# Performance work log

Hardware: AMD Instinct MI355X
Metric: run time of the kernel (lower is better)

The kernel has to match this reference:

```python
import jax, jax.numpy as jnp
import numpy as np

N_NODES = 50000
N_EDGES_UND = 400000
N_GRAPHS = 128
LATENT = 64
OUT_DIM = 64
NODE_F = 64
EDGE_F = 32
MAX_LV = 3


def setup_inputs() -> dict:
    key = jax.random.key(0)
    ks = jax.random.split(key, 12)
    rng = np.random.default_rng(0)
    # Build consistent directed edge list: each undirected pair (u,v) yields
    # directed edges e (u->v) and e+E_und (v->u); rev maps each to its twin.
    u = rng.integers(0, N_NODES, size=N_EDGES_UND)
    v = rng.integers(0, N_NODES, size=N_EDGES_UND)
    src = jnp.asarray(np.concatenate([u, v]), dtype=jnp.int32)
    dst = jnp.asarray(np.concatenate([v, u]), dtype=jnp.int32)
    e = np.arange(N_EDGES_UND)
    rev = jnp.asarray(np.concatenate([e + N_EDGES_UND, e]), dtype=jnp.int32)
    graph_ids = jnp.sort(jax.random.randint(ks[0], (N_NODES,), 0, N_GRAPHS)).astype(jnp.int32)
    s = 0.05
    return {
        'node_feat': jax.random.normal(ks[1], (N_NODES, NODE_F), jnp.float32),
        'edge_feat': jax.random.normal(ks[2], (2 * N_EDGES_UND, EDGE_F), jnp.float32),
        'src': src, 'dst': dst, 'rev': rev,
        'graph_ids': graph_ids, 'n_graphs': N_GRAPHS,
        'Wn': jax.random.normal(ks[3], (NODE_F, LATENT), jnp.float32) * s,
        'bn': jnp.zeros((LATENT,), jnp.float32),
        'We': jax.random.normal(ks[4], (EDGE_F, LATENT), jnp.float32) * s,
        'be': jnp.zeros((LATENT,), jnp.float32),
        'Wc': jax.random.normal(ks[5], (LATENT, LATENT), jnp.float32) * s,
        'bc': jnp.zeros((LATENT,), jnp.float32),
        'Wo': jax.random.normal(ks[6], (LATENT, OUT_DIM), jnp.float32) * s,
        'bo': jnp.zeros((OUT_DIM,), jnp.float32),
    }


def reference(node_feat, edge_feat, src, dst, rev, graph_ids, n_graphs,
              Wn, bn, We, be, Wc, bc, Wo, bo):
    n_nodes = node_feat.shape[0]
    # w_n2l / w_e2l
    input_node_linear = node_feat @ Wn + bn                  # [N, D]
    input_edge_linear = edge_feat @ We + be                  # [E, D]
    # n2e spmm: each directed edge gathers its source node's row
    input_message = input_edge_linear + input_node_linear[src]  # [E, D]
    cur = jax.nn.relu(input_message)
    # loopy BP: e2e spmm = (sum of messages into src node) - reverse-edge message
    for _ in range(MAX_LV):
        node_agg = jax.ops.segment_sum(cur, dst, num_segments=n_nodes)  # [N, D]
        e2epool = node_agg[src] - cur[rev]                              # [E, D]
        cur = jax.nn.relu(e2epool @ Wc + bc + input_message)
    # e2n spmm: sum incoming edge messages per node
    e2npool = jax.ops.segment_sum(cur, dst, num_segments=n_nodes)       # [N, D]
    hidden_msg = jax.nn.relu(e2npool)
    reluact = jax.nn.relu(hidden_msg @ Wo + bo)                         # [N, out]
    # subg spmm: sum node outputs per graph
    y = jax.ops.segment_sum(reluact, graph_ids, num_segments=n_graphs)  # [G, out]
    return jax.nn.relu(y)
```

## Files before the change

### kernel.cpp

```cpp
#include <hip/hip_runtime.h>


#define NN 50000
#define NE 800000
#define NG 128
#define D 64
#define LDE 36
#define LDW 66
#define LDO 72

typedef unsigned short u16;
typedef unsigned int u32;
typedef __bf16 bf16x8 __attribute__((ext_vector_type(8)));
typedef float f32x4 __attribute__((ext_vector_type(4)));
typedef short s16x2 __attribute__((ext_vector_type(2)));

__device__ __forceinline__ float b2f(u16 u){ u32 x=((u32)u)<<16; float f; __builtin_memcpy(&f,&x,4); return f; }
__device__ __forceinline__ u16 f2b(float f){ u32 x; __builtin_memcpy(&x,&f,4); x += 0x7fffu + ((x>>16)&1u); return (u16)(x>>16); }
__device__ __forceinline__ u32 pack2(float a, float b){ return (u32)f2b(a) | ((u32)f2b(b)<<16); }
__device__ __forceinline__ void unpack8(uint4 v, float* o){
  o[0]=b2f((u16)(v.x&0xffffu)); o[1]=b2f((u16)(v.x>>16));
  o[2]=b2f((u16)(v.y&0xffffu)); o[3]=b2f((u16)(v.y>>16));
  o[4]=b2f((u16)(v.z&0xffffu)); o[5]=b2f((u16)(v.z>>16));
  o[6]=b2f((u16)(v.w&0xffffu)); o[7]=b2f((u16)(v.w>>16));
}
__device__ __forceinline__ void atomic_pk_bf16(u16* addr, float lo, float hi){
  s16x2 v; v.x = (short)f2b(lo); v.y = (short)f2b(hi);
  __builtin_amdgcn_global_atomic_fadd_v2bf16((s16x2*)addr, v);
}

__global__ __launch_bounds__(256) void k_prep(const float* __restrict__ Wc, const float* __restrict__ We,
                                              u16* __restrict__ wcB, u16* __restrict__ weB){
  int i = blockIdx.x*256 + threadIdx.x;
  if (i < 4096){
    int nt = i>>10, r = i&1023;
    int h = r>>9, r2 = r&511;
    int j = r2>>3, kk = r2&7;
    int row = nt*16 + (j&15);
    int k = h*32 + (j>>4)*8 + kk;
    wcB[i] = f2b(Wc[k*D + row]);
  }
  int t = i - 4096;
  if (t >= 0 && t < 2048){
    int nt = t>>9, r = t&511;
    int j = r>>3, kk = r&7;
    int row = nt*16 + (j&15);
    int k = (j>>4)*8 + kk;
    weB[t] = f2b(We[k*D + row]);
  }
}

__global__ __launch_bounds__(256) void k_inl(const float* __restrict__ nf, const float* __restrict__ Wn,
                                             const float* __restrict__ bn, u16* __restrict__ inlb){
  __shared__ float w[D*D];
  for (int i=threadIdx.x;i<D*D;i+=256) w[i]=Wn[i];
  __syncthreads();
  const int d = threadIdx.x&63;
  const int n = blockIdx.x*4 + (threadIdx.x>>6);
  if (n>=NN) return;
  float v = bn[d];
  const float* row = nf + (size_t)n*D;
  #pragma unroll 8
  for (int k=0;k<D;k++) v += row[k]*w[k*D+d];
  inlb[(size_t)n*D+d] = f2b(v);
}

__global__ __launch_bounds__(256) void k_im(const float* __restrict__ ef, const u16* __restrict__ weB,
                                            const float* __restrict__ be, const u16* __restrict__ inlb,
                                            const int* __restrict__ src, const int* __restrict__ perm,
                                            u16* __restrict__ imP){
  __shared__ __align__(16) u16 efs[64*LDE];
  __shared__ float os[64*68];
  const int t = threadIdx.x;
  const int ebase = blockIdx.x*64;
  {
    int e=t>>2, k0=(t&3)*8;
    const float* p = ef + (size_t)(ebase+e)*32 + k0;
    float4 v0=*(const float4*)p, v1=*(const float4*)(p+4);
    uint4 pk = make_uint4(pack2(v0.x,v0.y),pack2(v0.z,v0.w),pack2(v1.x,v1.y),pack2(v1.z,v1.w));
    *(uint4*)&efs[e*LDE + k0] = pk;
  }
  {
    int w=t>>6, lane=t&63, q=lane>>4, mr=lane&15;
    int rowb=w*16;
    bf16x8 A = *(const bf16x8*)&efs[(rowb+mr)*LDE + q*8];
    #pragma unroll
    for (int nt=0;nt<4;nt++){
      bf16x8 B = *(const bf16x8*)(weB + nt*512 + lane*8);
      f32x4 acc = {0.f,0.f,0.f,0.f};
      acc = __builtin_amdgcn_mfma_f32_16x16x32_bf16(A,B,acc,0,0,0);
      #pragma unroll
      for (int r=0;r<4;r++) os[(rowb+q*4+r)*68 + nt*16+mr] = acc[r];
    }
  }
  {
    int e=t>>2, d0=(t&3)*16;
    const size_t eg = (size_t)(ebase+e);
    const int s = src[eg], ps = perm[eg];
    const u16* ip = inlb + (size_t)s*D + d0;
    uint4 iv0 = *(const uint4*)ip, iv1 = *(const uint4*)(ip+8);
    float il[16]; unpack8(iv0,il); unpack8(iv1,il+8);
    float x[16];
    #pragma unroll
    for (int j=0;j<16;j++) x[j] = os[e*68 + d0 + j] + be[d0+j] + il[j];
    uint4 p0 = make_uint4(pack2(x[0],x[1]),pack2(x[2],x[3]),pack2(x[4],x[5]),pack2(x[6],x[7]));
    uint4 p1 = make_uint4(pack2(x[8],x[9]),pack2(x[10],x[11]),pack2(x[12],x[13]),pack2(x[14],x[15]));
    u16* op = imP + (size_t)ps*D + d0;
    *(uint4*)op = p0; *(uint4*)(op+8) = p1;
  }
}

template<int MODE>
__global__ __launch_bounds__(256) void k_iter(const u16* __restrict__ imP, const u16* __restrict__ revIn,
      const u16* __restrict__ naWb, const u16* __restrict__ wcB, const float* __restrict__ bc,
      const int* __restrict__ srcP, const int* __restrict__ prevP, const int* __restrict__ nodeP,
      u16* __restrict__ revOut, u16* __restrict__ naWb_out){
  __shared__ __align__(16) u16 xs[64*LDW];
  __shared__ __align__(16) u16 os[64*LDO];
  __shared__ int nid[64];
  const int t = threadIdx.x;
  const int lane = t&63, w = t>>6;
  const size_t sbase = (size_t)blockIdx.x*64;
  if (lane < 16) nid[w*16 + lane] = nodeP[sbase + w*16 + lane];
  {
    const int e = t>>2, d0 = (t&3)*16;
    const size_t slot = sbase + e;
    const u16* ip = imP + slot*D + d0;
    uint4 r0 = *(const uint4*)ip, r1 = *(const uint4*)(ip+8);
    float x[16]; unpack8(r0,x); unpack8(r1,x+8);
    if (MODE == 1){
      const int sp = srcP[slot];
      const u16* cp = revIn + slot*D + d0;
      uint4 c0=*(const uint4*)cp, c1=*(const uint4*)(cp+8);
      const u16* np_ = naWb + (size_t)sp*D + d0;
      uint4 n0=*(const uint4*)np_, n1=*(const uint4*)(np_+8);
      float cv[16], nv[16];
      unpack8(c0,cv); unpack8(c1,cv+8);
      unpack8(n0,nv); unpack8(n1,nv+8);
      #pragma unroll
      for (int j=0;j<16;j++) x[j] += nv[j] - cv[j] + bc[d0+j];
    }
    #pragma unroll
    for (int j=0;j<16;j++) x[j] = x[j]>0.f ? x[j] : 0.f;
    uint4 p0 = make_uint4(pack2(x[0],x[1]),pack2(x[2],x[3]),pack2(x[4],x[5]),pack2(x[6],x[7]));
    uint4 p1 = make_uint4(pack2(x[8],x[9]),pack2(x[10],x[11]),pack2(x[12],x[13]),pack2(x[14],x[15]));
    u16* qd = &xs[e*LDW + d0];
    *(uint4*)qd = p0; *(uint4*)(qd+8) = p1;
  }
  {
    const int q = lane>>4, mr = lane&15;
    const int rowb = w*16;
    bf16x8 A0 = *(const bf16x8*)&xs[(rowb+mr)*LDW + q*8];
    bf16x8 A1 = *(const bf16x8*)&xs[(rowb+mr)*LDW + 32 + q*8];
    #pragma unroll
    for (int nt=0;nt<4;nt++){
      bf16x8 B0 = *(const bf16x8*)(wcB + nt*1024 + lane*8);
      bf16x8 B1 = *(const bf16x8*)(wcB + nt*1024 + 512 + lane*8);
      f32x4 acc = {0.f,0.f,0.f,0.f};
      acc = __builtin_amdgcn_mfma_f32_16x16x32_bf16(A0,B0,acc,0,0,0);
      acc = __builtin_amdgcn_mfma_f32_16x16x32_bf16(A1,B1,acc,0,0,0);
      #pragma unroll
      for (int r=0;r<4;r++) os[(rowb+q*4+r)*LDO + nt*16 + mr] = f2b(acc[r]);
    }
    const int lr = lane>>2, cc = lane&3;
    const int tgt = prevP[sbase + rowb + lr];
    u16* gp = revOut + (size_t)tgt*D + cc*16;
    *(uint4*)gp     = *(const uint4*)&os[(rowb+lr)*LDO + cc*16];
    *(uint4*)(gp+8) = *(const uint4*)&os[(rowb+lr)*LDO + cc*16 + 8];
    float acc = 0.f;
    int curn = nid[rowb];
    #pragma unroll 4
    for (int i=0;i<16;++i){
      int n = nid[rowb+i];
      if (n != curn){
        float hi = __shfl_xor(acc, 1, 64);
        if (!(lane&1)) atomic_pk_bf16(naWb_out + (size_t)curn*D + lane, acc, hi);
        curn = n; acc = 0.f;
      }
      acc += b2f(os[(rowb+i)*LDO + lane]);
    }
    float hi = __shfl_xor(acc, 1, 64);
    if (!(lane&1)) atomic_pk_bf16(naWb_out + (size_t)curn*D + lane, acc, hi);
  }
}

__global__ __launch_bounds__(256) void k_last(const u16* __restrict__ imP, const u16* __restrict__ revIn,
      const u16* __restrict__ naWb, const float* __restrict__ bc,
      const int* __restrict__ srcP, const int* __restrict__ nodeP,
      float* __restrict__ e2n){
  __shared__ __align__(16) u16 xs[64*LDW];
  __shared__ int nid[64];
  const int t = threadIdx.x;
  const int lane = t&63, w = t>>6;
  const size_t sbase = (size_t)blockIdx.x*64;
  if (lane < 16) nid[w*16+lane] = nodeP[sbase + w*16 + lane];
  {
    const int e = t>>2, d0 = (t&3)*16;
    const size_t slot = sbase + e;
    const u16* ip = imP + slot*D + d0;
    uint4 r0 = *(const uint4*)ip, r1 = *(const uint4*)(ip+8);
    float x[16]; unpack8(r0,x); unpack8(r1,x+8);
    const int sp = srcP[slot];
    const u16* cp = revIn + slot*D + d0;
    uint4 c0 = *(const uint4*)cp, c1 = *(const uint4*)(cp+8);
    const u16* np_ = naWb + (size_t)sp*D + d0;
    uint4 n0 = *(const uint4*)np_, n1 = *(const uint4*)(np_+8);
    float cv[16], nv[16];
    unpack8(c0,cv); unpack8(c1,cv+8);
    unpack8(n0,nv); unpack8(n1,nv+8);
    #pragma unroll
    for (int j=0;j<16;j++){ x[j] += nv[j] - cv[j] + bc[d0+j]; x[j] = x[j]>0.f ? x[j] : 0.f; }
    uint4 p0 = make_uint4(pack2(x[0],x[1]),pack2(x[2],x[3]),pack2(x[4],x[5]),pack2(x[6],x[7]));
    uint4 p1 = make_uint4(pack2(x[8],x[9]),pack2(x[10],x[11]),pack2(x[12],x[13]),pack2(x[14],x[15]));
    u16* qd = &xs[e*LDW + d0];
    *(uint4*)qd = p0; *(uint4*)(qd+8) = p1;
  }
  {
    float acc = 0.f;
    int curn = nid[w*16];
    #pragma unroll 4
    for (int i=0;i<16;++i){
      int n = nid[w*16+i];
      if (n != curn){
        atomicAdd(&e2n[(size_t)curn*D + lane], acc);
        curn = n; acc = 0.f;
      }
      acc += b2f(xs[(w*16+i)*LDW + lane]);
    }
    atomicAdd(&e2n[(size_t)curn*D + lane], acc);
  }
}

__global__ void k_hist(const int* __restrict__ dst, int* __restrict__ cnt){
  int e = blockIdx.x*256 + threadIdx.x;
  atomicAdd(&cnt[dst[e]], 1);
}
__global__ __launch_bounds__(1024) void k_scan1(const int* __restrict__ cnt, int* __restrict__ outv,
                                                int* __restrict__ bsums, int n){
  __shared__ int sh[1024];
  int i = blockIdx.x*1024 + threadIdx.x;
  int v = (i<n)? cnt[i] : 0;
  sh[threadIdx.x]=v;
  __syncthreads();
  for (int off=1; off<1024; off<<=1){
    int tv = (threadIdx.x>=(unsigned)off)? sh[threadIdx.x-off] : 0;
    __syncthreads();
    sh[threadIdx.x] += tv;
    __syncthreads();
  }
  if (i<n) outv[i] = sh[threadIdx.x] - v;
  if (threadIdx.x==1023) bsums[blockIdx.x] = sh[1023];
}
__global__ __launch_bounds__(1024) void k_scan3(int* __restrict__ off, int* __restrict__ cur,
                                                const int* __restrict__ bsums, int n){
  __shared__ int spref;
  if (threadIdx.x < 64){
    int v = ((int)threadIdx.x < (int)blockIdx.x) ? bsums[threadIdx.x] : 0;
    #pragma unroll
    for (int o=1;o<64;o<<=1) v += __shfl_xor(v, o, 64);
    if (threadIdx.x==0) spref = v;
  }
  __syncthreads();
  int i = blockIdx.x*1024 + threadIdx.x;
  if (i<n){ int v = off[i] + spref; off[i]=v; cur[i]=v; }
}
__global__ void k_fill(const int* __restrict__ dst, const int* __restrict__ src,
                       int* __restrict__ cur, int* __restrict__ perm,
                       int* __restrict__ srcP, int* __restrict__ nodeP){
  int e = blockIdx.x*256 + threadIdx.x;
  int d = dst[e];
  int pos = atomicAdd(&cur[d], 1);
  perm[e] = pos;
  srcP[pos] = src[e];
  nodeP[pos] = d;
}
__global__ void k_prev(const int* __restrict__ rev, const int* __restrict__ perm, int* __restrict__ prevP){
  int e = blockIdx.x*256 + threadIdx.x;
  prevP[perm[e]] = perm[rev[e]];
}

__global__ __launch_bounds__(256) void k_final(const float* __restrict__ e2n, const float* __restrict__ Wo,
                                               const float* __restrict__ bo, const int* __restrict__ gid,
                                               float* __restrict__ yacc){
  __shared__ float w[D*D];
  for (int i=threadIdx.x;i<D*D;i+=256) w[i]=Wo[i];
  __syncthreads();
  const int d = threadIdx.x&63, sub = threadIdx.x>>6;
  const int n0 = blockIdx.x*32 + sub*8;
  const float bod = bo[d];
  float acc=0.f; int curg=-1;
  for (int i=0;i<8;i++){
    int n=n0+i;
    if (n>=NN) break;
    int g = gid[n];
    if (g!=curg){ if (curg>=0) atomicAdd(&yacc[curg*D+d], acc); curg=g; acc=0.f; }
    float v=bod;
    const float* er = e2n + (size_t)n*D;
    #pragma unroll 8
    for (int k=0;k<D;k++){ float h=er[k]; h = h>0.f?h:0.f; v += h*w[k*D+d]; }
    acc += (v>0.f ? v : 0.f);
  }
  if (curg>=0) atomicAdd(&yacc[curg*D+d], acc);
}
__global__ void k_out(const float* __restrict__ yacc, float* __restrict__ outp){
  int i = blockIdx.x*256 + threadIdx.x;
  if (i<NG*D){ float v=yacc[i]; outp[i]= v>0.f?v:0.f; }
}

static constexpr size_t SZ_E   = (size_t)NE*D*2;
static constexpr size_t SZ_NF4 = (size_t)NN*D*4;
static constexpr size_t SZ_NB  = (size_t)NN*D*2;
static constexpr size_t OFF_IMP  = 0;
static constexpr size_t OFF_RVA  = SZ_E;
static constexpr size_t OFF_RVB  = 2*SZ_E;
static constexpr size_t OFF_CCUR = 3*SZ_E;
static constexpr size_t OFF_E2N  = OFF_CCUR + 200064;
static constexpr size_t OFF_YACC = OFF_E2N + SZ_NF4;
static constexpr size_t OFF_NB0  = OFF_YACC + (size_t)NG*D*4;
static constexpr size_t OFF_NB1  = OFF_NB0 + SZ_NB;
static constexpr size_t OFF_NB2  = OFF_NB1 + SZ_NB;
static constexpr size_t ZERO_SZ  = 200064 + SZ_NF4 + (size_t)NG*D*4 + 3*SZ_NB;
static constexpr size_t OFF_INL  = OFF_NB2 + SZ_NB;
static constexpr size_t OFF_COFF = OFF_INL + SZ_NB;
static constexpr size_t OFF_PERM = OFF_COFF + 200064;
static constexpr size_t OFF_SRCP = OFF_PERM + (size_t)NE*4;
static constexpr size_t OFF_PRVP = OFF_SRCP + (size_t)NE*4;
static constexpr size_t OFF_NODP = OFF_PRVP + (size_t)NE*4;
static constexpr size_t OFF_BS   = OFF_NODP + (size_t)NE*4;
static constexpr size_t OFF_WCT  = OFF_BS + 256;
static constexpr size_t OFF_WET  = OFF_WCT + 8192;

extern "C" void kernel_launch(void* const* d_in, const int* in_sizes, int n_in,
                              void* d_out, int out_size, void* d_ws, size_t ws_size,
                              hipStream_t stream) {
  const float* node_feat = (const float*)d_in[0];
  const float* edge_feat = (const float*)d_in[1];
  const int*   src       = (const int*)d_in[2];
  const int*   dst       = (const int*)d_in[3];
  const int*   rev       = (const int*)d_in[4];
  const int*   gid       = (const int*)d_in[5];
  const float* Wn = (const float*)d_in[7];
  const float* bn = (const float*)d_in[8];
  const float* We = (const float*)d_in[9];
  const float* be = (const float*)d_in[10];
  const float* Wc = (const float*)d_in[11];
  const float* bc = (const float*)d_in[12];
  const float* Wo = (const float*)d_in[13];
  const float* bo = (const float*)d_in[14];

  char* ws = (char*)d_ws;
  u16*   imP     = (u16*)(ws + OFF_IMP);
  u16*   revA    = (u16*)(ws + OFF_RVA);
  u16*   revB    = (u16*)(ws + OFF_RVB);
  float* e2n     = (float*)(ws + OFF_E2N);
  float* yacc    = (float*)(ws + OFF_YACC);
  u16*   nb0     = (u16*)(ws + OFF_NB0);
  u16*   nb1     = (u16*)(ws + OFF_NB1);
  u16*   nb2     = (u16*)(ws + OFF_NB2);
  u16*   inlb    = (u16*)(ws + OFF_INL);
  int*   csr_off = (int*)(ws + OFF_COFF);
  int*   csr_cur = (int*)(ws + OFF_CCUR);
  int*   perm    = (int*)(ws + OFF_PERM);
  int*   srcP    = (int*)(ws + OFF_SRCP);
  int*   prevP   = (int*)(ws + OFF_PRVP);
  int*   nodeP   = (int*)(ws + OFF_NODP);
  int*   bsums   = (int*)(ws + OFF_BS);
  u16*   wcB     = (u16*)(ws + OFF_WCT);
  u16*   weB     = (u16*)(ws + OFF_WET);

  hipMemsetAsync(ws + OFF_CCUR, 0, ZERO_SZ, stream);

  k_hist <<<NE/256, 256, 0, stream>>>(dst, csr_cur);
  k_scan1<<<49, 1024, 0, stream>>>(csr_cur, csr_off, bsums, NN);
  k_scan3<<<49, 1024, 0, stream>>>(csr_off, csr_cur, bsums, NN);
  k_fill <<<NE/256, 256, 0, stream>>>(dst, src, csr_cur, perm, srcP, nodeP);
  k_prev <<<NE/256, 256, 0, stream>>>(rev, perm, prevP);

  k_prep<<<24, 256, 0, stream>>>(Wc, We, wcB, weB);
  k_inl <<<NN/4, 256, 0, stream>>>(node_feat, Wn, bn, inlb);
  k_im  <<<NE/64, 256, 0, stream>>>(edge_feat, weB, be, inlb, src, perm, imP);

  k_iter<0><<<NE/64, 256, 0, stream>>>(imP, revA, nb0, wcB, bc, srcP, prevP, nodeP, revA, nb0);
  k_iter<1><<<NE/64, 256, 0, stream>>>(imP, revA, nb0, wcB, bc, srcP, prevP, nodeP, revB, nb1);
  k_iter<1><<<NE/64, 256, 0, stream>>>(imP, revB, nb1, wcB, bc, srcP, prevP, nodeP, revA, nb2);
  k_last<<<NE/64, 256, 0, stream>>>(imP, revA, nb2, bc, srcP, nodeP, e2n);

  k_final<<<(NN+31)/32, 256, 0, stream>>>(e2n, Wo, bo, gid, yacc);
  k_out<<<(NG*D)/256, 256, 0, stream>>>(yacc, (float*)d_out);
}
```

Baseline: 649.4 us.

## Fuse prep kernels, use bf16 e2n atomics, and MFMA final projection

Merges the histogram, weight-conversion and node-linear kernels into one launch by splitting on block index, and adds a bf16 Wo layout for MFMA. The last iteration now accumulates e2n with packed bf16 atomics instead of fp32 atomics, which halves that buffer and its memset. The final projection uses MFMA on 64-node tiles instead of scalar FMA loops. This cuts launch count and memory traffic, at the cost of precision in the e2n sum, since bf16 atomic accumulation loses accuracy.

```diff
diff --git a/kernel.cpp b/kernel.cpp
--- a/kernel.cpp
+++ b/kernel.cpp
@@ -29,35 +29,51 @@
   __builtin_amdgcn_global_atomic_fadd_v2bf16((s16x2*)addr, v);
 }
 
-__global__ __launch_bounds__(256) void k_prep(const float* __restrict__ Wc, const float* __restrict__ We,
-                                              u16* __restrict__ wcB, u16* __restrict__ weB){
-  int i = blockIdx.x*256 + threadIdx.x;
-  if (i < 4096){
-    int nt = i>>10, r = i&1023;
-    int h = r>>9, r2 = r&511;
-    int j = r2>>3, kk = r2&7;
-    int row = nt*16 + (j&15);
-    int k = h*32 + (j>>4)*8 + kk;
-    wcB[i] = f2b(Wc[k*D + row]);
-  }
-  int t = i - 4096;
-  if (t >= 0 && t < 2048){
-    int nt = t>>9, r = t&511;
-    int j = r>>3, kk = r&7;
-    int row = nt*16 + (j&15);
-    int k = (j>>4)*8 + kk;
-    weB[t] = f2b(We[k*D + row]);
-  }
-}
-
-__global__ __launch_bounds__(256) void k_inl(const float* __restrict__ nf, const float* __restrict__ Wn,
-                                             const float* __restrict__ bn, u16* __restrict__ inlb){
+__global__ __launch_bounds__(256) void k_pi0(const float* __restrict__ nf, const float* __restrict__ Wn,
+                                             const float* __restrict__ bn, const float* __restrict__ Wc,
+                                             const float* __restrict__ We, const float* __restrict__ Wo,
+                                             const int* __restrict__ dst,
+                                             u16* __restrict__ inlb, u16* __restrict__ wcB,
+                                             u16* __restrict__ weB, u16* __restrict__ woB,
+                                             int* __restrict__ cnt){
+  const int bid = blockIdx.x;
+  if (bid >= 12540){
+    int e = (bid - 12540)*256 + threadIdx.x;
+    atomicAdd(&cnt[dst[e]], 1);
+    return;
+  }
+  if (bid >= 12500){
+    int i = (bid - 12500)*256 + threadIdx.x;
+    if (i < 4096){
+      int nt = i>>10, r = i&1023;
+      int h = r>>9, r2 = r&511;
+      int j = r2>>3, kk = r2&7;
+      int row = nt*16 + (j&15);
+      int k = h*32 + (j>>4)*8 + kk;
+      wcB[i] = f2b(Wc[k*D + row]);
+    } else if (i < 6144){
+      int t = i - 4096;
+      int nt = t>>9, r = t&511;
+      int j = r>>3, kk = r&7;
+      int row = nt*16 + (j&15);
+      int k = (j>>4)*8 + kk;
+      weB[t] = f2b(We[k*D + row]);
+    } else if (i < 10240){
+      int t = i - 6144;
+      int nt = t>>10, r = t&1023;
+      int h = r>>9, r2 = r&511;
+      int j = r2>>3, kk = r2&7;
+      int row = nt*16 + (j&15);
+      int k = h*32 + (j>>4)*8 + kk;
+      woB[t] = f2b(Wo[k*D + row]);
+    }
+    return;
+  }
   __shared__ float w[D*D];
   for (int i=threadIdx.x;i<D*D;i+=256) w[i]=Wn[i];
   __syncthreads();
   const int d = threadIdx.x&63;
-  const int n = blockIdx.x*4 + (threadIdx.x>>6);
-  if (n>=NN) return;
+  const int n = bid*4 + (threadIdx.x>>6);
   float v = bn[d];
   const float* row = nf + (size_t)n*D;
   #pragma unroll 8
@@ -187,7 +203,7 @@
 __global__ __launch_bounds__(256) void k_last(const u16* __restrict__ imP, const u16* __restrict__ revIn,
       const u16* __restrict__ naWb, const float* __restrict__ bc,
       const int* __restrict__ srcP, const int* __restrict__ nodeP,
-      float* __restrict__ e2n){
+      u16* __restrict__ e2nb){
   __shared__ __align__(16) u16 xs[64*LDW];
   __shared__ int nid[64];
   const int t = threadIdx.x;
@@ -222,19 +238,17 @@
     for (int i=0;i<16;++i){
       int n = nid[w*16+i];
       if (n != curn){
-        atomicAdd(&e2n[(size_t)curn*D + lane], acc);
+        float hi = __shfl_xor(acc, 1, 64);
+        if (!(lane&1)) atomic_pk_bf16(e2nb + (size_t)curn*D + lane, acc, hi);
         curn = n; acc = 0.f;
       }
       acc += b2f(xs[(w*16+i)*LDW + lane]);
     }
-    atomicAdd(&e2n[(size_t)curn*D + lane], acc);
-  }
-}
-
-__global__ void k_hist(const int* __restrict__ dst, int* __restrict__ cnt){
-  int e = blockIdx.x*256 + threadIdx.x;
-  atomicAdd(&cnt[dst[e]], 1);
-}
+    float hi = __shfl_xor(acc, 1, 64);
+    if (!(lane&1)) atomic_pk_bf16(e2nb + (size_t)curn*D + lane, acc, hi);
+  }
+}
+
 __global__ __launch_bounds__(1024) void k_scan1(const int* __restrict__ cnt, int* __restrict__ outv,
                                                 int* __restrict__ bsums, int n){
   __shared__ int sh[1024];
@@ -279,28 +293,70 @@
   prevP[perm[e]] = perm[rev[e]];
 }
 
-__global__ __launch_bounds__(256) void k_final(const float* __restrict__ e2n, const float* __restrict__ Wo,
-                                               const float* __restrict__ bo, const int* __restrict__ gid,
-                                               float* __restrict__ yacc){
-  __shared__ float w[D*D];
-  for (int i=threadIdx.x;i<D*D;i+=256) w[i]=Wo[i];
-  __syncthreads();
-  const int d = threadIdx.x&63, sub = threadIdx.x>>6;
-  const int n0 = blockIdx.x*32 + sub*8;
-  const float bod = bo[d];
-  float acc=0.f; int curg=-1;
-  for (int i=0;i<8;i++){
-    int n=n0+i;
-    if (n>=NN) break;
-    int g = gid[n];
-    if (g!=curg){ if (curg>=0) atomicAdd(&yacc[curg*D+d], acc); curg=g; acc=0.f; }
-    float v=bod;
-    const float* er = e2n + (size_t)n*D;
-    #pragma unroll 8
-    for (int k=0;k<D;k++){ float h=er[k]; h = h>0.f?h:0.f; v += h*w[k*D+d]; }
-    acc += (v>0.f ? v : 0.f);
-  }
-  if (curg>=0) atomicAdd(&yacc[curg*D+d], acc);
+__global__ __launch_bounds__(256) void k_finalM(const u16* __restrict__ e2nb, const u16* __restrict__ woB,
+                                                const float* __restrict__ bo, const int* __restrict__ gid,
+                                                float* __restrict__ yacc){
+  __shared__ __align__(16) u16 xs[64*LDW];
+  __shared__ float os[64*68];
+  __shared__ int gidS[64];
+  const int t = threadIdx.x;
+  const int lane = t&63, w = t>>6;
+  const int nbase = blockIdx.x*64;
+  if (lane < 16){
+    int n = nbase + w*16 + lane;
+    gidS[w*16 + lane] = (n < NN) ? gid[n] : -1;
+  }
+  {
+    const int e = t>>2, d0 = (t&3)*16;
+    const int n = nbase + e;
+    float x[16];
+    if (n < NN){
+      const u16* ip = e2nb + (size_t)n*D + d0;
+      uint4 r0 = *(const uint4*)ip, r1 = *(const uint4*)(ip+8);
+      unpack8(r0,x); unpack8(r1,x+8);
+      #pragma unroll
+      for (int j=0;j<16;j++) x[j] = x[j]>0.f ? x[j] : 0.f;
+    } else {
+      #pragma unroll
+      for (int j=0;j<16;j++) x[j] = 0.f;
+    }
+    uint4 p0 = make_uint4(pack2(x[0],x[1]),pack2(x[2],x[3]),pack2(x[4],x[5]),pack2(x[6],x[7]));
+    uint4 p1 = make_uint4(pack2(x[8],x[9]),pack2(x[10],x[11]),pack2(x[12],x[13]),pack2(x[14],x[15]));
+    u16* qd = &xs[e*LDW + d0];
+    *(uint4*)qd = p0; *(uint4*)(qd+8) = p1;
+  }
+  {
+    const int q = lane>>4, mr = lane&15;
+    const int rowb = w*16;
+    bf16x8 A0 = *(const bf16x8*)&xs[(rowb+mr)*LDW + q*8];
+    bf16x8 A1 = *(const bf16x8*)&xs[(rowb+mr)*LDW + 32 + q*8];
+    #pragma unroll
+    for (int nt=0;nt<4;nt++){
+      bf16x8 B0 = *(const bf16x8*)(woB + nt*1024 + lane*8);
+      bf16x8 B1 = *(const bf16x8*)(woB + nt*1024 + 512 + lane*8);
+      f32x4 acc = {0.f,0.f,0.f,0.f};
+      acc = __builtin_amdgcn_mfma_f32_16x16x32_bf16(A0,B0,acc,0,0,0);
+      acc = __builtin_amdgcn_mfma_f32_16x16x32_bf16(A1,B1,acc,0,0,0);
+      #pragma unroll
+      for (int r=0;r<4;r++) os[(rowb+q*4+r)*68 + nt*16 + mr] = acc[r];
+    }
+    const float bol = bo[lane];
+    float acc = 0.f;
+    int curg = gidS[rowb];
+    #pragma unroll 4
+    for (int i=0;i<16;++i){
+      int g = gidS[rowb+i];
+      if (g != curg){
+        if (curg >= 0) atomicAdd(&yacc[curg*D + lane], acc);
+        curg = g; acc = 0.f;
+      }
+      if (g >= 0){
+        float v = os[(rowb+i)*68 + lane] + bol;
+        acc += v>0.f ? v : 0.f;
+      }
+    }
+    if (curg >= 0) atomicAdd(&yacc[curg*D + lane], acc);
+  }
 }
 __global__ void k_out(const float* __restrict__ yacc, float* __restrict__ outp){
   int i = blockIdx.x*256 + threadIdx.x;
@@ -308,19 +364,18 @@
 }
 
 static constexpr size_t SZ_E   = (size_t)NE*D*2;
-static constexpr size_t SZ_NF4 = (size_t)NN*D*4;
 static constexpr size_t SZ_NB  = (size_t)NN*D*2;
 static constexpr size_t OFF_IMP  = 0;
 static constexpr size_t OFF_RVA  = SZ_E;
 static constexpr size_t OFF_RVB  = 2*SZ_E;
 static constexpr size_t OFF_CCUR = 3*SZ_E;
-static constexpr size_t OFF_E2N  = OFF_CCUR + 200064;
-static constexpr size_t OFF_YACC = OFF_E2N + SZ_NF4;
+static constexpr size_t OFF_YACC = OFF_CCUR + 200064;
 static constexpr size_t OFF_NB0  = OFF_YACC + (size_t)NG*D*4;
 static constexpr size_t OFF_NB1  = OFF_NB0 + SZ_NB;
 static constexpr size_t OFF_NB2  = OFF_NB1 + SZ_NB;
-static constexpr size_t ZERO_SZ  = 200064 + SZ_NF4 + (size_t)NG*D*4 + 3*SZ_NB;
-static constexpr size_t OFF_INL  = OFF_NB2 + SZ_NB;
+static constexpr size_t OFF_E2NB = OFF_NB2 + SZ_NB;
+static constexpr size_t ZERO_SZ  = 200064 + (size_t)NG*D*4 + 4*SZ_NB;
+static constexpr size_t OFF_INL  = OFF_E2NB + SZ_NB;
 static constexpr size_t OFF_COFF = OFF_INL + SZ_NB;
 static constexpr size_t OFF_PERM = OFF_COFF + 200064;
 static constexpr size_t OFF_SRCP = OFF_PERM + (size_t)NE*4;
@@ -329,6 +384,7 @@
 static constexpr size_t OFF_BS   = OFF_NODP + (size_t)NE*4;
 static constexpr size_t OFF_WCT  = OFF_BS + 256;
 static constexpr size_t OFF_WET  = OFF_WCT + 8192;
+static constexpr size_t OFF_WOT  = OFF_WET + 4096;
 
 extern "C" void kernel_launch(void* const* d_in, const int* in_sizes, int n_in,
                               void* d_out, int out_size, void* d_ws, size_t ws_size,
@@ -352,11 +408,11 @@
   u16*   imP     = (u16*)(ws + OFF_IMP);
   u16*   revA    = (u16*)(ws + OFF_RVA);
   u16*   revB    = (u16*)(ws + OFF_RVB);
-  float* e2n     = (float*)(ws + OFF_E2N);
   float* yacc    = (float*)(ws + OFF_YACC);
   u16*   nb0     = (u16*)(ws + OFF_NB0);
   u16*   nb1     = (u16*)(ws + OFF_NB1);
   u16*   nb2     = (u16*)(ws + OFF_NB2);
+  u16*   e2nb    = (u16*)(ws + OFF_E2NB);
   u16*   inlb    = (u16*)(ws + OFF_INL);
   int*   csr_off = (int*)(ws + OFF_COFF);
   int*   csr_cur = (int*)(ws + OFF_CCUR);
@@ -367,24 +423,24 @@
   int*   bsums   = (int*)(ws + OFF_BS);
   u16*   wcB     = (u16*)(ws + OFF_WCT);
   u16*   weB     = (u16*)(ws + OFF_WET);
+  u16*   woB     = (u16*)(ws + OFF_WOT);
 
   hipMemsetAsync(ws + OFF_CCUR, 0, ZERO_SZ, stream);
 
-  k_hist <<<NE/256, 256, 0, stream>>>(dst, csr_cur);
+  k_pi0<<<15665, 256, 0, stream>>>(node_feat, Wn, bn, Wc, We, Wo, dst, inlb, wcB, weB, woB, csr_cur);
+
   k_scan1<<<49, 1024, 0, stream>>>(csr_cur, csr_off, bsums, NN);
   k_scan3<<<49, 1024, 0, stream>>>(csr_off, csr_cur, bsums, NN);
   k_fill <<<NE/256, 256, 0, stream>>>(dst, src, csr_cur, perm, srcP, nodeP);
   k_prev <<<NE/256, 256, 0, stream>>>(rev, perm, prevP);
 
-  k_prep<<<24, 256, 0, stream>>>(Wc, We, wcB, weB);
-  k_inl <<<NN/4, 256, 0, stream>>>(node_feat, Wn, bn, inlb);
   k_im  <<<NE/64, 256, 0, stream>>>(edge_feat, weB, be, inlb, src, perm, imP);
 
   k_iter<0><<<NE/64, 256, 0, stream>>>(imP, revA, nb0, wcB, bc, srcP, prevP, nodeP, revA, nb0);
   k_iter<1><<<NE/64, 256, 0, stream>>>(imP, revA, nb0, wcB, bc, srcP, prevP, nodeP, revB, nb1);
   k_iter<1><<<NE/64, 256, 0, stream>>>(imP, revB, nb1, wcB, bc, srcP, prevP, nodeP, revA, nb2);
-  k_last<<<NE/64, 256, 0, stream>>>(imP, revA, nb2, bc, srcP, nodeP, e2n);
-
-  k_final<<<(NN+31)/32, 256, 0, stream>>>(e2n, Wo, bo, gid, yacc);
+  k_last<<<NE/64, 256, 0, stream>>>(imP, revA, nb2, bc, srcP, nodeP, e2nb);
+
+  k_finalM<<<(NN+63)/64, 256, 0, stream>>>(e2nb, woB, bo, gid, yacc);
   k_out<<<(NG*D)/256, 256, 0, stream>>>(yacc, (float*)d_out);
 }
```

Result: faster. 613.2 us (-5.6%).
